# Kernel optimization log

Hardware: AMD Instinct MI355X
Metric: run time of the kernel (lower is better)

## Reference

```python
import jax, jax.numpy as jnp
import numpy as np

GROUPS = 32
EPS = 1e-5


def setup_inputs() -> dict:
    key = jax.random.key(0)
    ks = jax.random.split(key, 11)
    B, C, H, W = 64, 256, 32, 32
    s = 1.0 / np.sqrt(C)  # conv1d k=1 init scale
    inp = {
        'x': jax.random.normal(ks[0], (B, C, H, W), jnp.float32),
        'gn_weight': jnp.ones((C,), jnp.float32),
        'gn_bias': jnp.zeros((C,), jnp.float32),
        'wq': jax.random.uniform(ks[1], (C, C), jnp.float32, -s, s),
        'bq': jax.random.uniform(ks[2], (C,), jnp.float32, -s, s),
        'wk': jax.random.uniform(ks[3], (C, C), jnp.float32, -s, s),
        'bk': jax.random.uniform(ks[4], (C,), jnp.float32, -s, s),
        'wv': jax.random.uniform(ks[5], (C, C), jnp.float32, -s, s),
        'bv': jax.random.uniform(ks[6], (C,), jnp.float32, -s, s),
        'wo': jax.random.uniform(ks[7], (C, C), jnp.float32, -s, s),
        'bo': jax.random.uniform(ks[8], (C,), jnp.float32, -s, s),
    }
    return inp


def _group_norm(x, weight, bias):
    # x: (B, C, H, W); normalize per (group-channels, H, W)
    B, C, H, W = x.shape
    xg = x.reshape(B, GROUPS, C // GROUPS, H, W)
    mean = xg.mean(axis=(2, 3, 4), keepdims=True)
    var = xg.var(axis=(2, 3, 4), keepdims=True)
    xg = (xg - mean) * jax.lax.rsqrt(var + EPS)
    xn = xg.reshape(B, C, H, W)
    return xn * weight[None, :, None, None] + bias[None, :, None, None]


def reference(x, gn_weight, gn_bias, wq, bq, wk, bk, wv, bv, wo, bo):
    B, C, H, W = x.shape
    h = _group_norm(x, gn_weight, gn_bias).reshape(B, C, H * W)  # (B,C,N)
    # 1x1 conv1d == per-position linear over channels
    q = jnp.einsum('oc,bcn->bon', wq, h) + bq[None, :, None]
    k = jnp.einsum('oc,bcn->bon', wk, h) + bk[None, :, None]
    v = jnp.einsum('oc,bcn->bon', wv, h) + bv[None, :, None]
    scores = jnp.einsum('bcn,bcm->bnm', q, k) * (C ** -0.5)  # (B,N,N)
    weights = jax.nn.softmax(scores, axis=-1)
    attn = jnp.einsum('bnm,bcm->bcn', weights, v)  # (B,C,N)
    out = jnp.einsum('oc,bcn->bon', wo, attn) + bo[None, :, None]
    return x + out.reshape(B, C, H, W)
```

## Files before the change

### kernel.cpp

```cpp
#include <hip/hip_runtime.h>


#define BB 64
#define CC 256
#define NN 1024

typedef float  floatx4  __attribute__((ext_vector_type(4)));
typedef short  shortx8  __attribute__((ext_vector_type(8)));
typedef unsigned short ushortx4 __attribute__((ext_vector_type(4)));
typedef unsigned short ushortx8 __attribute__((ext_vector_type(8)));

__device__ __forceinline__ unsigned short f2bf(float f) {
  union { float f; unsigned int u; } cv; cv.f = f;
  unsigned int u = cv.u;
  u += 0x7fffu + ((u >> 16) & 1u);
  return (unsigned short)(u >> 16);
}

__device__ __forceinline__ unsigned int cvtpk(float lo, float hi) {
  unsigned int r;
  asm("v_cvt_pk_bf16_f32 %0, %1, %2" : "=v"(r) : "v"(lo), "v"(hi));
  return r;
}

__device__ __forceinline__ floatx4 mfma16(shortx8 a, shortx8 b, floatx4 c) {
  return __builtin_amdgcn_mfma_f32_16x16x32_bf16(a, b, c, 0, 0, 0);
}

__device__ __forceinline__ void gload16(const unsigned short* g, unsigned short* s) {
  __builtin_amdgcn_global_load_lds(
      reinterpret_cast<const __attribute__((address_space(1))) void*>(
          (unsigned long long)g),
      reinterpret_cast<__attribute__((address_space(3))) void*>(
          (unsigned int)(unsigned long long)s),
      16, 0, 0);
}

__device__ __forceinline__ void barrier_raw() {
  asm volatile("" ::: "memory");
  __builtin_amdgcn_s_barrier();
  asm volatile("" ::: "memory");
}

__device__ __forceinline__ void bar_lds() {
  asm volatile("s_waitcnt lgkmcnt(0)" ::: "memory");
  __builtin_amdgcn_sched_barrier(0);
  barrier_raw();
}

__device__ __forceinline__ int sigma32(int r) {
  return (((r >> 2) & 3) << 3) + (((r >> 4) & 1) << 2) + (r & 3);
}

__global__ void convert_w(const float* __restrict__ wq, const float* __restrict__ bq,
                          const float* __restrict__ wk, const float* __restrict__ bk,
                          const float* __restrict__ wv, const float* __restrict__ bv,
                          const float* __restrict__ wo,
                          unsigned short* __restrict__ wqkv,
                          unsigned short* __restrict__ wo_bf,
                          float* __restrict__ bqkv) {
  const float QS = 0.0625f * 1.44269504088896f;
  int i = blockIdx.x * 256 + threadIdx.x;
  if (i < 196608) {
    int o = i >> 8, c = i & 255;
    float val;
    if (o < 256)      val = wq[o * 256 + c] * QS;
    else if (o < 512) val = wk[(o - 256) * 256 + c];
    else              val = wv[(o - 512) * 256 + c];
    wqkv[i] = f2bf(val);
  } else if (i < 262144) {
    int j = i - 196608;
    wo_bf[j] = f2bf(wo[j]);
  } else if (i < 262912) {
    int o = i - 262144;
    float val;
    if (o < 256)      val = bq[o] * QS;
    else if (o < 512) val = bk[o - 256];
    else              val = bv[o - 512];
    bqkv[o] = val;
  }
}

__global__ __launch_bounds__(256) void gn_kernel(const float* __restrict__ x,
                                                 const float* __restrict__ gw,
                                                 const float* __restrict__ gb,
                                                 unsigned short* __restrict__ h_t) {
  int g = blockIdx.x, b = blockIdx.y;
  int t = threadIdx.x;
  const float* xb = x + ((size_t)b * CC + g * 8) * NN;

  float vals[8][4];
  float s = 0.f, sq = 0.f;
#pragma unroll
  for (int cc = 0; cc < 8; cc++) {
    floatx4 v4 = *(const floatx4*)(xb + cc * NN + t * 4);
#pragma unroll
    for (int j = 0; j < 4; j++) {
      vals[cc][j] = v4[j];
      s += v4[j];
      sq += v4[j] * v4[j];
    }
  }
#pragma unroll
  for (int d = 1; d < 64; d <<= 1) {
    s  += __shfl_xor(s, d);
    sq += __shfl_xor(sq, d);
  }
  __shared__ float ssum[4], ssq[4];
  int w = t >> 6;
  if ((t & 63) == 0) { ssum[w] = s; ssq[w] = sq; }
  __syncthreads();
  s  = ssum[0] + ssum[1] + ssum[2] + ssum[3];
  sq = ssq[0] + ssq[1] + ssq[2] + ssq[3];
  float mean = s * (1.f / 8192.f);
  float var  = sq * (1.f / 8192.f) - mean * mean;
  float rstd = rsqrtf(var + 1e-5f);

  float gam[8], bet[8];
#pragma unroll
  for (int cc = 0; cc < 8; cc++) {
    float gm = gw[g * 8 + cc] * rstd;
    gam[cc] = gm;
    bet[cc] = gb[g * 8 + cc] - mean * gm;
  }
  unsigned short* hb = h_t + (size_t)b * NN * CC + g * 8;
#pragma unroll
  for (int j = 0; j < 4; j++) {
    ushortx8 pk;
#pragma unroll
    for (int cc = 0; cc < 8; cc++) pk[cc] = f2bf(vals[cc][j] * gam[cc] + bet[cc]);
    *(ushortx8*)(hb + (size_t)(t * 4 + j) * CC) = pk;
  }
}

__global__ __launch_bounds__(512, 4) void qkv_gemm(const unsigned short* __restrict__ h_t,
                                                   const unsigned short* __restrict__ wqkv,
                                                   const float* __restrict__ bqkv,
                                                   unsigned short* __restrict__ q_t,
                                                   unsigned short* __restrict__ k_t,
                                                   unsigned short* __restrict__ v) {
  __shared__ __align__(16) unsigned short sM[32768];
  __shared__ __align__(16) unsigned short sRep[32 * 136];
  int rb = blockIdx.x, b = blockIdx.y;
  int t = threadIdx.x, w = t >> 6, l = t & 63, lo = l & 15, h = l >> 4;
  int rowg = w >> 1, colg = w & 1;
  const unsigned short* A = h_t + ((size_t)b * NN + rb * 128) * CC;

  int srow_w = w * 2 + (l >> 5);
  int schunk = l & 31;

#pragma unroll
  for (int i = 0; i < 8; i++) {
    int row = i * 16 + srow_w;
    gload16(A + (size_t)row * CC + ((schunk ^ (row & 7)) << 3),
            &sM[(i * 16 + w * 2) << 8]);
  }
  asm volatile("s_waitcnt vmcnt(0)" ::: "memory");
  barrier_raw();

  shortx8 a[2][8];
#pragma unroll
  for (int i = 0; i < 2; i++) {
    int row = rowg * 32 + i * 16 + lo;
#pragma unroll
    for (int ch = 0; ch < 8; ch++)
      a[i][ch] = *(const shortx8*)(&sM[(row << 8) + (((ch * 4 + h) ^ (row & 7)) << 3)]);
  }
  bar_lds();

#pragma unroll
  for (int i = 0; i < 4; i++) {
    int row = i * 16 + srow_w;
    gload16(wqkv + (size_t)row * CC + ((schunk ^ (row & 7)) << 3),
            &sM[(i * 16 + w * 2) << 8]);
  }

  floatx4 zero4 = {0.f, 0.f, 0.f, 0.f};
  for (int c = 0; c < 12; c++) {
    int cb = (c & 1) << 14;
    if (c < 11) {
      int nb = ((c + 1) & 1) << 14;
#pragma unroll
      for (int i = 0; i < 4; i++) {
        int row = i * 16 + srow_w;
        gload16(wqkv + (size_t)((c + 1) * 64 + row) * CC + ((schunk ^ (row & 7)) << 3),
                &sM[nb + ((i * 16 + w * 2) << 8)]);
      }
      asm volatile("s_waitcnt vmcnt(4)" ::: "memory");
    } else {
      asm volatile("s_waitcnt vmcnt(0)" ::: "memory");
    }
    barrier_raw();

    floatx4 acc[2][2];
    acc[0][0] = zero4; acc[0][1] = zero4; acc[1][0] = zero4; acc[1][1] = zero4;
    int r0 = colg * 32 + lo, r1 = colg * 32 + 16 + lo;
    __builtin_amdgcn_s_setprio(1);
#pragma unroll
    for (int ch = 0; ch < 8; ch++) {
      shortx8 b0 = *(const shortx8*)(&sM[cb + (r0 << 8) + (((ch * 4 + h) ^ (r0 & 7)) << 3)]);
      shortx8 b1 = *(const shortx8*)(&sM[cb + (r1 << 8) + (((ch * 4 + h) ^ (r1 & 7)) << 3)]);
      acc[0][0] = mfma16(a[0][ch], b0, acc[0][0]);
      acc[0][1] = mfma16(a[0][ch], b1, acc[0][1]);
      acc[1][0] = mfma16(a[1][ch], b0, acc[1][0]);
      acc[1][1] = mfma16(a[1][ch], b1, acc[1][1]);
    }
    __builtin_amdgcn_s_setprio(0);

    if (c < 8) {
      unsigned short* dst = (c < 4) ? q_t : k_t;
      int oc0 = ((c & 3) << 6) + colg * 32;
#pragma unroll
      for (int i = 0; i < 2; i++) {
#pragma unroll
        for (int j = 0; j < 2; j++) {
          float bias = bqkv[(c << 6) + colg * 32 + j * 16 + lo];
#pragma unroll
          for (int r = 0; r < 4; r++) {
            int n = rb * 128 + rowg * 32 + i * 16 + h * 4 + r;
            dst[((size_t)b * NN + n) * CC + oc0 + j * 16 + lo] = f2bf(acc[i][j][r] + bias);
          }
        }
      }
      bar_lds();
    } else {
      int vch0 = (c - 8) << 6;
#pragma unroll
      for (int half = 0; half < 2; half++) {
        if (colg == half) {
#pragma unroll
          for (int i = 0; i < 2; i++) {
#pragma unroll
            for (int j = 0; j < 2; j++) {
              float bias = bqkv[512 + vch0 + half * 32 + j * 16 + lo];
              ushortx4 pk;
#pragma unroll
              for (int r = 0; r < 4; r++) pk[r] = f2bf(acc[i][j][r] + bias);
              *(ushortx4*)(&sRep[(j * 16 + lo) * 136 + rowg * 32 + i * 16 + h * 4]) = pk;
            }
          }
        }
        bar_lds();
        int o_l = t >> 4, nseg = (t & 15) << 3;
        ushortx8 vv = *(const ushortx8*)(&sRep[o_l * 136 + nseg]);
        *(ushortx8*)(v + ((size_t)b * CC + vch0 + half * 32 + o_l) * NN + rb * 128 + nseg) = vv;
        bar_lds();
      }
    }
  }
}

__global__ __launch_bounds__(256, 2) void flash_kernel(const unsigned short* __restrict__ q_t,
                                                       const unsigned short* __restrict__ k_t,
                                                       const unsigned short* __restrict__ v,
                                                       unsigned short* __restrict__ attn_t) {
  __shared__ __align__(16) unsigned short sMem[32768];
  int bid = blockIdx.x;
  int wgid = ((bid & 7) << 6) + (bid >> 3);
  int b = wgid >> 3, qblk = wgid & 7;
  int t = threadIdx.x, w = t >> 6, l = t & 63, lo = l & 15, h = l >> 4;
  const unsigned short* qtb = q_t + (size_t)b * NN * CC;
  const unsigned short* ktb = k_t + (size_t)b * NN * CC;
  const unsigned short* vb  = v   + (size_t)b * CC * NN;
  int qbase = qblk * 128 + w * 32;

  shortx8 qfA[8], qfB[8];
#pragma unroll
  for (int ch = 0; ch < 8; ch++) {
    qfA[ch] = *(const shortx8*)(qtb + (size_t)(qbase + lo) * CC + ch * 32 + h * 8);
    qfB[ch] = *(const shortx8*)(qtb + (size_t)(qbase + 16 + lo) * CC + ch * 32 + h * 8);
  }

  floatx4 zero4 = {0.f, 0.f, 0.f, 0.f};
  floatx4 oA[16], oB[16];
#pragma unroll
  for (int i = 0; i < 16; i++) { oA[i] = zero4; oB[i] = zero4; }
  float mA = -1e30f, lsA = 0.f, mB = -1e30f, lsB = 0.f;

  int krow_l = (w << 3) + (l >> 5);
  int kchunk = l & 31;
  int vrow_l = (w << 6) + (l >> 2);
  int vchunk = l & 3;

#pragma unroll
  for (int i = 0; i < 4; i++) {
    int row = krow_l + i * 2;
    gload16(ktb + (size_t)sigma32(row) * CC + ((kchunk ^ (row & 7)) << 3),
            &sMem[((w << 3) + i * 2) << 8]);
  }
#pragma unroll
  for (int i = 0; i < 4; i++) {
    int row = vrow_l + i * 16;
    gload16(vb + (size_t)row * NN + ((vchunk ^ ((row >> 1) & 3)) << 3),
            &sMem[16384 + (((w << 6) + i * 16) << 5)]);
  }

  for (int kb = 0; kb < 32; kb++) {
    int cur = kb & 1;
    int kB = cur << 13;
    int vB = 16384 + (cur << 13);
    if (kb < 31) {
      int nxt = cur ^ 1, k0n = (kb + 1) << 5;
#pragma unroll
      for (int i = 0; i < 4; i++) {
        int row = krow_l + i * 2;
        gload16(ktb + (size_t)(k0n + sigma32(row)) * CC + ((kchunk ^ (row & 7)) << 3),
                &sMem[(nxt << 13) + (((w << 3) + i * 2) << 8)]);
      }
#pragma unroll
      for (int i = 0; i < 4; i++) {
        int row = vrow_l + i * 16;
        gload16(vb + (size_t)row * NN + k0n + ((vchunk ^ ((row >> 1) & 3)) << 3),
                &sMem[16384 + (nxt << 13) + (((w << 6) + i * 16) << 5)]);
      }
      asm volatile("s_waitcnt vmcnt(8)" ::: "memory");
    } else {
      asm volatile("s_waitcnt vmcnt(0)" ::: "memory");
    }
    barrier_raw();

    floatx4 sA[2], sB[2];
#pragma unroll
    for (int i = 0; i < 2; i++) { sA[i] = zero4; sB[i] = zero4; }
    __builtin_amdgcn_s_setprio(1);
#pragma unroll
    for (int kt = 0; kt < 2; kt++) {
      const unsigned short* kp = &sMem[kB + ((kt * 16 + lo) << 8)];
#pragma unroll
      for (int ch = 0; ch < 8; ch++) {
        shortx8 kf = *(const shortx8*)(kp + (((ch * 4 + h) ^ (lo & 7)) << 3));
        sA[kt] = mfma16(kf, qfA[ch], sA[kt]);
        sB[kt] = mfma16(kf, qfB[ch], sB[kt]);
      }
    }
    __builtin_amdgcn_s_setprio(0);

    unsigned int pkA[2][2], pkB[2][2];
    {
      float t1 = fmaxf(fmaxf(sA[0][0], sA[0][1]), sA[0][2]);
      float t2 = fmaxf(fmaxf(sA[0][3], sA[1][0]), sA[1][1]);
      float t3 = fmaxf(fmaxf(sA[1][2], sA[1][3]), t1);
      float pmax = fmaxf(t2, t3);
      if (!__all(pmax - mA <= 8.f)) {
        pmax = fmaxf(pmax, __shfl_xor(pmax, 16));
        pmax = fmaxf(pmax, __shfl_xor(pmax, 32));
        float mn = fmaxf(mA, pmax);
        float alpha = exp2f(mA - mn);
        mA = mn;
        lsA *= alpha;
#pragma unroll
        for (int r = 0; r < 4; r++) {
          float ar = __shfl(alpha, (h << 4) + (h << 2) + r);
#pragma unroll
          for (int cbi = 0; cbi < 16; cbi++) oA[cbi][r] *= ar;
        }
      }
      float rs = 0.f;
#pragma unroll
      for (int kt = 0; kt < 2; kt++) {
        float p0 = exp2f(sA[kt][0] - mA);
        float p1 = exp2f(sA[kt][1] - mA);
        float p2 = exp2f(sA[kt][2] - mA);
        float p3 = exp2f(sA[kt][3] - mA);
        rs += (p0 + p1) + (p2 + p3);
        pkA[kt][0] = cvtpk(p0, p1);
        pkA[kt][1] = cvtpk(p2, p3);
      }
      lsA += rs;
    }
    {
      float t1 = fmaxf(fmaxf(sB[0][0], sB[0][1]), sB[0][2]);
      float t2 = fmaxf(fmaxf(sB[0][3], sB[1][0]), sB[1][1]);
      float t3 = fmaxf(fmaxf(sB[1][2], sB[1][3]), t1);
      float pmax = fmaxf(t2, t3);
      if (!__all(pmax - mB <= 8.f)) {
        pmax = fmaxf(pmax, __shfl_xor(pmax, 16));
        pmax = fmaxf(pmax, __shfl_xor(pmax, 32));
        float mn = fmaxf(mB, pmax);
        float alpha = exp2f(mB - mn);
        mB = mn;
        lsB *= alpha;
#pragma unroll
        for (int r = 0; r < 4; r++) {
          float ar = __shfl(alpha, (h << 4) + (h << 2) + r);
#pragma unroll
          for (int cbi = 0; cbi < 16; cbi++) oB[cbi][r] *= ar;
        }
      }
      float rs = 0.f;
#pragma unroll
      for (int kt = 0; kt < 2; kt++) {
        float p0 = exp2f(sB[kt][0] - mB);
        float p1 = exp2f(sB[kt][1] - mB);
        float p2 = exp2f(sB[kt][2] - mB);
        float p3 = exp2f(sB[kt][3] - mB);
        rs += (p0 + p1) + (p2 + p3);
        pkB[kt][0] = cvtpk(p0, p1);
        pkB[kt][1] = cvtpk(p2, p3);
      }
      lsB += rs;
    }

    {
      union { unsigned int u[4]; shortx8 v; } paA, paB;
      paA.u[0] = pkA[0][0]; paA.u[1] = pkA[0][1];
      paA.u[2] = pkA[1][0]; paA.u[3] = pkA[1][1];
      paB.u[0] = pkB[0][0]; paB.u[1] = pkB[0][1];
      paB.u[2] = pkB[1][0]; paB.u[3] = pkB[1][1];
      __builtin_amdgcn_s_setprio(1);
#pragma unroll
      for (int cbi = 0; cbi < 16; cbi++) {
        int row = (cbi << 4) + lo;
        shortx8 vf = *(const shortx8*)(&sMem[vB + (row << 5) +
                                             ((h ^ ((row >> 1) & 3)) << 3)]);
        oA[cbi] = mfma16(paA.v, vf, oA[cbi]);
        oB[cbi] = mfma16(paB.v, vf, oB[cbi]);
      }
      __builtin_amdgcn_s_setprio(0);
    }
    barrier_raw();
  }

  lsA += __shfl_xor(lsA, 16);
  lsA += __shfl_xor(lsA, 32);
  lsB += __shfl_xor(lsB, 16);
  lsB += __shfl_xor(lsB, 32);

  float rlA[4], rlB[4];
#pragma unroll
  for (int r = 0; r < 4; r++) {
    rlA[r] = 1.f / __shfl(lsA, (h << 4) + (h << 2) + r);
    rlB[r] = 1.f / __shfl(lsB, (h << 4) + (h << 2) + r);
  }
  unsigned short* ab = attn_t + (size_t)b * NN * CC;
  unsigned short* ow = &sMem[w << 12];

#pragma unroll
  for (int cbi = 0; cbi < 16; cbi++) {
#pragma unroll
    for (int r = 0; r < 4; r++) {
      int q = (h << 2) + r;
      int c = (cbi << 4) + lo;
      int sw = (q ^ (q >> 3)) & 7;
      ow[(q << 8) + (((c >> 3) ^ sw) << 3) + (lo & 7)] = f2bf(oA[cbi][r] * rlA[r]);
    }
  }
  bar_lds();
#pragma unroll
  for (int it = 0; it < 8; it++) {
    int q = (it << 1) + (l >> 5);
    int gc = l & 31;
    int sw = (q ^ (q >> 3)) & 7;
    ushortx8 vv = *(const ushortx8*)(&ow[(q << 8) + ((gc ^ sw) << 3)]);
    *(ushortx8*)(ab + (size_t)(qbase + q) * CC + (gc << 3)) = vv;
  }
  bar_lds();
#pragma unroll
  for (int cbi = 0; cbi < 16; cbi++) {
#pragma unroll
    for (int r = 0; r < 4; r++) {
      int q = (h << 2) + r;
      int c = (cbi << 4) + lo;
      int sw = (q ^ (q >> 3)) & 7;
      ow[(q << 8) + (((c >> 3) ^ sw) << 3) + (lo & 7)] = f2bf(oB[cbi][r] * rlB[r]);
    }
  }
  bar_lds();
#pragma unroll
  for (int it = 0; it < 8; it++) {
    int q = (it << 1) + (l >> 5);
    int gc = l & 31;
    int sw = (q ^ (q >> 3)) & 7;
    ushortx8 vv = *(const ushortx8*)(&ow[(q << 8) + ((gc ^ sw) << 3)]);
    *(ushortx8*)(ab + (size_t)(qbase + 16 + q) * CC + (gc << 3)) = vv;
  }
}

__global__ __launch_bounds__(512, 4) void outproj_gemm(const unsigned short* __restrict__ attn_t,
                                                       const unsigned short* __restrict__ wo_bf,
                                                       const float* __restrict__ bo,
                                                       const float* __restrict__ x,
                                                       float* __restrict__ out) {
  __shared__ __align__(16) unsigned short sM[32768];
  __shared__ __align__(16) float sRepF[16 * 132];
  int rb = blockIdx.x, b = blockIdx.y;
  int t = threadIdx.x, w = t >> 6, l = t & 63, lo = l & 15, h = l >> 4;
  int rowg = w >> 1, colg = w & 1;
  const unsigned short* A = attn_t + ((size_t)b * NN + rb * 128) * CC;

  int srow_w = w * 2 + (l >> 5);
  int schunk = l & 31;

#pragma unroll
  for (int i = 0; i < 8; i++) {
    int row = i * 16 + srow_w;
    gload16(A + (size_t)row * CC + ((schunk ^ (row & 7)) << 3),
            &sM[(i * 16 + w * 2) << 8]);
  }
  asm volatile("s_waitcnt vmcnt(0)" ::: "memory");
  barrier_raw();

  shortx8 a[2][8];
#pragma unroll
  for (int i = 0; i < 2; i++) {
    int row = rowg * 32 + i * 16 + lo;
#pragma unroll
    for (int ch = 0; ch < 8; ch++)
      a[i][ch] = *(const shortx8*)(&sM[(row << 8) + (((ch * 4 + h) ^ (row & 7)) << 3)]);
  }
  bar_lds();

#pragma unroll
  for (int i = 0; i < 4; i++) {
    int row = i * 16 + srow_w;
    gload16(wo_bf + (size_t)row * CC + ((schunk ^ (row & 7)) << 3),
            &sM[(i * 16 + w * 2) << 8]);
  }

  floatx4 zero4 = {0.f, 0.f, 0.f, 0.f};
  for (int c = 0; c < 4; c++) {
    int cb = (c & 1) << 14;
    if (c < 3) {
      int nb = ((c + 1) & 1) << 14;
#pragma unroll
      for (int i = 0; i < 4; i++) {
        int row = i * 16 + srow_w;
        gload16(wo_bf + (size_t)((c + 1) * 64 + row) * CC + ((schunk ^ (row & 7)) << 3),
                &sM[nb + ((i * 16 + w * 2) << 8)]);
      }
      asm volatile("s_waitcnt vmcnt(4)" ::: "memory");
    } else {
      asm volatile("s_waitcnt vmcnt(0)" ::: "memory");
    }
    barrier_raw();

    floatx4 acc[2][2];
    acc[0][0] = zero4; acc[0][1] = zero4; acc[1][0] = zero4; acc[1][1] = zero4;
    int r0 = colg * 32 + lo, r1 = colg * 32 + 16 + lo;
    __builtin_amdgcn_s_setprio(1);
#pragma unroll
    for (int ch = 0; ch < 8; ch++) {
      shortx8 b0 = *(const shortx8*)(&sM[cb + (r0 << 8) + (((ch * 4 + h) ^ (r0 & 7)) << 3)]);
      shortx8 b1 = *(const shortx8*)(&sM[cb + (r1 << 8) + (((ch * 4 + h) ^ (r1 & 7)) << 3)]);
      acc[0][0] = mfma16(a[0][ch], b0, acc[0][0]);
      acc[0][1] = mfma16(a[0][ch], b1, acc[0][1]);
      acc[1][0] = mfma16(a[1][ch], b0, acc[1][0]);
      acc[1][1] = mfma16(a[1][ch], b1, acc[1][1]);
    }
    __builtin_amdgcn_s_setprio(0);

#pragma unroll
    for (int quarter = 0; quarter < 4; quarter++) {
      int j = quarter & 1;
      if (colg == (quarter >> 1)) {
        float bias = bo[(c << 6) + quarter * 16 + lo];
#pragma unroll
        for (int i = 0; i < 2; i++) {
          floatx4 val;
#pragma unroll
          for (int r = 0; r < 4; r++) val[r] = acc[i][j][r] + bias;
          *(floatx4*)(&sRepF[lo * 132 + rowg * 32 + i * 16 + h * 4]) = val;
        }
      }
      bar_lds();
      int o_l = t >> 5, nq = (t & 31) << 2;
      floatx4 rep = *(const floatx4*)(&sRepF[o_l * 132 + nq]);
      size_t idx = ((size_t)b * CC + (c << 6) + quarter * 16 + o_l) * NN + rb * 128 + nq;
      floatx4 xr = *(const floatx4*)(x + idx);
#pragma unroll
      for (int r = 0; r < 4; r++) rep[r] += xr[r];
      *(floatx4*)(out + idx) = rep;
      bar_lds();
    }
  }
}

extern "C" void kernel_launch(void* const* d_in, const int* in_sizes, int n_in,
                              void* d_out, int out_size, void* d_ws, size_t ws_size,
                              hipStream_t stream) {
  const float* x  = (const float*)d_in[0];
  const float* gw = (const float*)d_in[1];
  const float* gb = (const float*)d_in[2];
  const float* wq = (const float*)d_in[3];
  const float* bq = (const float*)d_in[4];
  const float* wk = (const float*)d_in[5];
  const float* bk = (const float*)d_in[6];
  const float* wv = (const float*)d_in[7];
  const float* bv = (const float*)d_in[8];
  const float* wo = (const float*)d_in[9];
  const float* bo = (const float*)d_in[10];
  float* out = (float*)d_out;

  char* ws = (char*)d_ws;
  unsigned short* q_t   = (unsigned short*)(ws);
  unsigned short* k_t   = (unsigned short*)(ws + 33554432);
  unsigned short* v     = (unsigned short*)(ws + 67108864);
  unsigned short* h_t   = (unsigned short*)(ws + 100663296);
  unsigned short* wqkv  = (unsigned short*)(ws + 134217728);
  unsigned short* wo_bf = (unsigned short*)(ws + 134610944);
  float*          bqkv  = (float*)(ws + 134742016);
  unsigned short* attn_t = h_t;

  convert_w<<<dim3(1027), dim3(256), 0, stream>>>(wq, bq, wk, bk, wv, bv, wo, wqkv, wo_bf, bqkv);
  gn_kernel<<<dim3(32, 64), dim3(256), 0, stream>>>(x, gw, gb, h_t);
  qkv_gemm<<<dim3(8, 64), dim3(512), 0, stream>>>(h_t, wqkv, bqkv, q_t, k_t, v);
  flash_kernel<<<dim3(512), dim3(256), 0, stream>>>(q_t, k_t, v, attn_t);
  outproj_gemm<<<dim3(8, 64), dim3(512), 0, stream>>>(attn_t, wo_bf, bo, x, out);
}
```

Before: 215.3 us.

## Software-pipeline flash attention so PV of previous tile overlaps next QK

Restructures the flash attention loop so each iteration issues the QK^T MFMAs for the current key tile together with the PV MFMAs for the previous tile's probabilities, leaving the softmax of the current tile to run after both. A prologue computes the first tile's softmax and an epilogue performs the final PV. V gets a triple-buffered LDS ring (LDS grows from 64KB to 80KB) so the previous V tile stays resident while the next one loads. The aim is to hide softmax exp/max latency behind matrix work. The cost is more LDS per block, which may reduce occupancy at 2 blocks per CU, and higher register pressure from carrying the packed probabilities across iterations.

New measurement: 259.4 us. +20.5%, slower.

```diff
diff --git a/kernel.cpp b/kernel.cpp
--- a/kernel.cpp
+++ b/kernel.cpp
@@ -254,7 +254,7 @@
                                                        const unsigned short* __restrict__ k_t,
                                                        const unsigned short* __restrict__ v,
                                                        unsigned short* __restrict__ attn_t) {
-  __shared__ __align__(16) unsigned short sMem[32768];
+  __shared__ __align__(16) unsigned short sMem[40960];
   int bid = blockIdx.x;
   int wgid = ((bid & 7) << 6) + (bid >> 3);
   int b = wgid >> 3, qblk = wgid & 7;
@@ -276,6 +276,7 @@
 #pragma unroll
   for (int i = 0; i < 16; i++) { oA[i] = zero4; oB[i] = zero4; }
   float mA = -1e30f, lsA = 0.f, mB = -1e30f, lsB = 0.f;
+  unsigned int ppA[4], ppB[4];
 
   int krow_l = (w << 3) + (l >> 5);
   int kchunk = l & 31;
@@ -283,49 +284,34 @@
   int vchunk = l & 3;
 
 #pragma unroll
-  for (int i = 0; i < 4; i++) {
-    int row = krow_l + i * 2;
-    gload16(ktb + (size_t)sigma32(row) * CC + ((kchunk ^ (row & 7)) << 3),
-            &sMem[((w << 3) + i * 2) << 8]);
-  }
-#pragma unroll
-  for (int i = 0; i < 4; i++) {
-    int row = vrow_l + i * 16;
-    gload16(vb + (size_t)row * NN + ((vchunk ^ ((row >> 1) & 3)) << 3),
-            &sMem[16384 + (((w << 6) + i * 16) << 5)]);
-  }
-
-  for (int kb = 0; kb < 32; kb++) {
-    int cur = kb & 1;
-    int kB = cur << 13;
-    int vB = 16384 + (cur << 13);
-    if (kb < 31) {
-      int nxt = cur ^ 1, k0n = (kb + 1) << 5;
-#pragma unroll
-      for (int i = 0; i < 4; i++) {
-        int row = krow_l + i * 2;
-        gload16(ktb + (size_t)(k0n + sigma32(row)) * CC + ((kchunk ^ (row & 7)) << 3),
-                &sMem[(nxt << 13) + (((w << 3) + i * 2) << 8)]);
-      }
-#pragma unroll
-      for (int i = 0; i < 4; i++) {
-        int row = vrow_l + i * 16;
-        gload16(vb + (size_t)row * NN + k0n + ((vchunk ^ ((row >> 1) & 3)) << 3),
-                &sMem[16384 + (nxt << 13) + (((w << 6) + i * 16) << 5)]);
-      }
-      asm volatile("s_waitcnt vmcnt(8)" ::: "memory");
-    } else {
-      asm volatile("s_waitcnt vmcnt(0)" ::: "memory");
-    }
-    barrier_raw();
-
+  for (int tt = 0; tt < 2; tt++) {
+    int k0 = tt << 5;
+    int kBufB = tt * 8192;
+    int vBufB = 16384 + tt * 8192;
+#pragma unroll
+    for (int i = 0; i < 4; i++) {
+      int row = krow_l + i * 2;
+      gload16(ktb + (size_t)(k0 + sigma32(row)) * CC + ((kchunk ^ (row & 7)) << 3),
+              &sMem[kBufB + (((w << 3) + i * 2) << 8)]);
+    }
+#pragma unroll
+    for (int i = 0; i < 4; i++) {
+      int row = vrow_l + i * 16;
+      gload16(vb + (size_t)row * NN + k0 + ((vchunk ^ ((row >> 1) & 3)) << 3),
+              &sMem[vBufB + (((w << 6) + i * 16) << 5)]);
+    }
+  }
+  asm volatile("s_waitcnt vmcnt(8)" ::: "memory");
+  barrier_raw();
+
+  {
     floatx4 sA[2], sB[2];
 #pragma unroll
     for (int i = 0; i < 2; i++) { sA[i] = zero4; sB[i] = zero4; }
     __builtin_amdgcn_s_setprio(1);
 #pragma unroll
     for (int kt = 0; kt < 2; kt++) {
-      const unsigned short* kp = &sMem[kB + ((kt * 16 + lo) << 8)];
+      const unsigned short* kp = &sMem[(kt * 16 + lo) << 8];
 #pragma unroll
       for (int ch = 0; ch < 8; ch++) {
         shortx8 kf = *(const shortx8*)(kp + (((ch * 4 + h) ^ (lo & 7)) << 3));
@@ -334,8 +320,107 @@
       }
     }
     __builtin_amdgcn_s_setprio(0);
-
-    unsigned int pkA[2][2], pkB[2][2];
+    {
+      float t1 = fmaxf(fmaxf(sA[0][0], sA[0][1]), sA[0][2]);
+      float t2 = fmaxf(fmaxf(sA[0][3], sA[1][0]), sA[1][1]);
+      float t3 = fmaxf(fmaxf(sA[1][2], sA[1][3]), t1);
+      float pmax = fmaxf(t2, t3);
+      pmax = fmaxf(pmax, __shfl_xor(pmax, 16));
+      pmax = fmaxf(pmax, __shfl_xor(pmax, 32));
+      mA = pmax;
+      float rs = 0.f;
+#pragma unroll
+      for (int kt = 0; kt < 2; kt++) {
+        float p0 = exp2f(sA[kt][0] - mA);
+        float p1 = exp2f(sA[kt][1] - mA);
+        float p2 = exp2f(sA[kt][2] - mA);
+        float p3 = exp2f(sA[kt][3] - mA);
+        rs += (p0 + p1) + (p2 + p3);
+        ppA[kt * 2 + 0] = cvtpk(p0, p1);
+        ppA[kt * 2 + 1] = cvtpk(p2, p3);
+      }
+      lsA = rs;
+    }
+    {
+      float t1 = fmaxf(fmaxf(sB[0][0], sB[0][1]), sB[0][2]);
+      float t2 = fmaxf(fmaxf(sB[0][3], sB[1][0]), sB[1][1]);
+      float t3 = fmaxf(fmaxf(sB[1][2], sB[1][3]), t1);
+      float pmax = fmaxf(t2, t3);
+      pmax = fmaxf(pmax, __shfl_xor(pmax, 16));
+      pmax = fmaxf(pmax, __shfl_xor(pmax, 32));
+      mB = pmax;
+      float rs = 0.f;
+#pragma unroll
+      for (int kt = 0; kt < 2; kt++) {
+        float p0 = exp2f(sB[kt][0] - mB);
+        float p1 = exp2f(sB[kt][1] - mB);
+        float p2 = exp2f(sB[kt][2] - mB);
+        float p3 = exp2f(sB[kt][3] - mB);
+        rs += (p0 + p1) + (p2 + p3);
+        ppB[kt * 2 + 0] = cvtpk(p0, p1);
+        ppB[kt * 2 + 1] = cvtpk(p2, p3);
+      }
+      lsB = rs;
+    }
+  }
+  barrier_raw();
+
+  int vStage = 2;
+  int vPV = 0;
+
+  for (int kb = 1; kb < 32; kb++) {
+    if (kb < 31) {
+      int k0n = (kb + 1) << 5;
+      int kBufN = ((kb + 1) & 1) * 8192;
+      int vBufN = 16384 + vStage * 8192;
+#pragma unroll
+      for (int i = 0; i < 4; i++) {
+        int row = krow_l + i * 2;
+        gload16(ktb + (size_t)(k0n + sigma32(row)) * CC + ((kchunk ^ (row & 7)) << 3),
+                &sMem[kBufN + (((w << 3) + i * 2) << 8)]);
+      }
+#pragma unroll
+      for (int i = 0; i < 4; i++) {
+        int row = vrow_l + i * 16;
+        gload16(vb + (size_t)row * NN + k0n + ((vchunk ^ ((row >> 1) & 3)) << 3),
+                &sMem[vBufN + (((w << 6) + i * 16) << 5)]);
+      }
+      asm volatile("s_waitcnt vmcnt(8)" ::: "memory");
+    } else {
+      asm volatile("s_waitcnt vmcnt(0)" ::: "memory");
+    }
+    barrier_raw();
+
+    int kB = (kb & 1) << 13;
+    int vB = 16384 + vPV * 8192;
+
+    floatx4 sA[2], sB[2];
+#pragma unroll
+    for (int i = 0; i < 2; i++) { sA[i] = zero4; sB[i] = zero4; }
+    union { unsigned int u[4]; shortx8 v; } paA, paB;
+    paA.u[0] = ppA[0]; paA.u[1] = ppA[1]; paA.u[2] = ppA[2]; paA.u[3] = ppA[3];
+    paB.u[0] = ppB[0]; paB.u[1] = ppB[1]; paB.u[2] = ppB[2]; paB.u[3] = ppB[3];
+    __builtin_amdgcn_s_setprio(1);
+#pragma unroll
+    for (int kt = 0; kt < 2; kt++) {
+      const unsigned short* kp = &sMem[kB + ((kt * 16 + lo) << 8)];
+#pragma unroll
+      for (int ch = 0; ch < 8; ch++) {
+        shortx8 kf = *(const shortx8*)(kp + (((ch * 4 + h) ^ (lo & 7)) << 3));
+        sA[kt] = mfma16(kf, qfA[ch], sA[kt]);
+        sB[kt] = mfma16(kf, qfB[ch], sB[kt]);
+      }
+    }
+#pragma unroll
+    for (int cbi = 0; cbi < 16; cbi++) {
+      int row = (cbi << 4) + lo;
+      shortx8 vf = *(const shortx8*)(&sMem[vB + (row << 5) +
+                                           ((h ^ ((row >> 1) & 3)) << 3)]);
+      oA[cbi] = mfma16(paA.v, vf, oA[cbi]);
+      oB[cbi] = mfma16(paB.v, vf, oB[cbi]);
+    }
+    __builtin_amdgcn_s_setprio(0);
+
     {
       float t1 = fmaxf(fmaxf(sA[0][0], sA[0][1]), sA[0][2]);
       float t2 = fmaxf(fmaxf(sA[0][3], sA[1][0]), sA[1][1]);
@@ -363,8 +448,8 @@
         float p2 = exp2f(sA[kt][2] - mA);
         float p3 = exp2f(sA[kt][3] - mA);
         rs += (p0 + p1) + (p2 + p3);
-        pkA[kt][0] = cvtpk(p0, p1);
-        pkA[kt][1] = cvtpk(p2, p3);
+        ppA[kt * 2 + 0] = cvtpk(p0, p1);
+        ppA[kt * 2 + 1] = cvtpk(p2, p3);
       }
       lsA += rs;
     }
@@ -395,30 +480,32 @@
         float p2 = exp2f(sB[kt][2] - mB);
         float p3 = exp2f(sB[kt][3] - mB);
         rs += (p0 + p1) + (p2 + p3);
-        pkB[kt][0] = cvtpk(p0, p1);
-        pkB[kt][1] = cvtpk(p2, p3);
+        ppB[kt * 2 + 0] = cvtpk(p0, p1);
+        ppB[kt * 2 + 1] = cvtpk(p2, p3);
       }
       lsB += rs;
     }
 
-    {
-      union { unsigned int u[4]; shortx8 v; } paA, paB;
-      paA.u[0] = pkA[0][0]; paA.u[1] = pkA[0][1];
-      paA.u[2] = pkA[1][0]; paA.u[3] = pkA[1][1];
-      paB.u[0] = pkB[0][0]; paB.u[1] = pkB[0][1];
-      paB.u[2] = pkB[1][0]; paB.u[3] = pkB[1][1];
-      __builtin_amdgcn_s_setprio(1);
-#pragma unroll
-      for (int cbi = 0; cbi < 16; cbi++) {
-        int row = (cbi << 4) + lo;
-        shortx8 vf = *(const shortx8*)(&sMem[vB + (row << 5) +
-                                             ((h ^ ((row >> 1) & 3)) << 3)]);
-        oA[cbi] = mfma16(paA.v, vf, oA[cbi]);
-        oB[cbi] = mfma16(paB.v, vf, oB[cbi]);
-      }
-      __builtin_amdgcn_s_setprio(0);
-    }
     barrier_raw();
+    vStage = (vStage == 2) ? 0 : vStage + 1;
+    vPV    = (vPV    == 2) ? 0 : vPV + 1;
+  }
+
+  {
+    int vB = 16384 + vPV * 8192;
+    union { unsigned int u[4]; shortx8 v; } paA, paB;
+    paA.u[0] = ppA[0]; paA.u[1] = ppA[1]; paA.u[2] = ppA[2]; paA.u[3] = ppA[3];
+    paB.u[0] = ppB[0]; paB.u[1] = ppB[1]; paB.u[2] = ppB[2]; paB.u[3] = ppB[3];
+    __builtin_amdgcn_s_setprio(1);
+#pragma unroll
+    for (int cbi = 0; cbi < 16; cbi++) {
+      int row = (cbi << 4) + lo;
+      shortx8 vf = *(const shortx8*)(&sMem[vB + (row << 5) +
+                                           ((h ^ ((row >> 1) & 3)) << 3)]);
+      oA[cbi] = mfma16(paA.v, vf, oA[cbi]);
+      oB[cbi] = mfma16(paB.v, vf, oB[cbi]);
+    }
+    __builtin_amdgcn_s_setprio(0);
   }
 
   lsA += __shfl_xor(lsA, 16);
```
